# Kernel optimization log

Hardware: AMD Instinct MI355X
Metric: run time of the kernel (lower is better)

## Reference

```python
import jax, jax.numpy as jnp
import numpy as np

N = 8192
D_IN = 3
D_K = 128
HID = 256
N_RES = 2
N_TRI = 2730
N_EDGE = 2048
EPS = float(jnp.finfo(jnp.float32).eps)  # torch RMSNorm default eps=None -> finfo eps


def setup_inputs() -> dict:
    key = jax.random.key(0)
    ks = jax.random.split(key, 16)
    std = 0.02
    inp = {
        "edge_features": jax.random.normal(ks[0], (N, D_IN), dtype=jnp.float32),
        "edge_ids": jax.random.randint(ks[1], (N,), 0, N_EDGE),
        "triangle_ids": jax.random.randint(ks[2], (N,), 0, N_TRI),
        # projections (stored as [in, out]; equivalent to torch Linear)
        "Wq": jax.random.normal(ks[3], (D_IN, D_K), dtype=jnp.float32) * std,
        "bq": jnp.zeros((D_K,), jnp.float32),
        "Wk": jax.random.normal(ks[4], (D_IN, D_K), dtype=jnp.float32) * std,
        "bk": jnp.zeros((D_K,), jnp.float32),
        "Wv": jax.random.normal(ks[5], (D_IN, D_K), dtype=jnp.float32) * std,
        "bv": jnp.zeros((D_K,), jnp.float32),
        # attention MLP: Linear(d_k, hid) -> N_RES ResBlocks -> Linear(hid, 1)
        "W0": jax.random.normal(ks[6], (D_K, HID), dtype=jnp.float32) * std,
        "b0": jnp.zeros((HID,), jnp.float32),
        "rms_w": jnp.ones((N_RES, HID), jnp.float32),
        "Wres": jax.random.normal(ks[7], (N_RES, HID, HID), dtype=jnp.float32) * std,
        "bres": jnp.zeros((N_RES, HID), jnp.float32),
        "Wout": jax.random.normal(ks[8], (HID, 1), dtype=jnp.float32) * std,
        "bout": jnp.zeros((1,), jnp.float32),
    }
    return inp


def _rmsnorm(x, g):
    ms = jnp.mean(x * x, axis=-1, keepdims=True)
    return x * jax.lax.rsqrt(ms + EPS) * g


def reference(edge_features, edge_ids, triangle_ids,
              Wq, bq, Wk, bk, Wv, bv,
              W0, b0, rms_w, Wres, bres, Wout, bout):
    q = edge_features @ Wq + bq          # [N, d_k]
    k = edge_features @ Wk + bk
    v = edge_features @ Wv + bv
    scores = (q @ k.T) / jnp.sqrt(jnp.float32(D_K))   # [N, N]
    mask = triangle_ids[:, None] == triangle_ids[None, :]
    scores = jnp.where(mask, scores, -jnp.inf)
    attn = jax.nn.softmax(scores, axis=1)             # every row has diag True
    attended = attn @ v                                # [N, d_k]
    # MLP with ResBlocks
    h = attended @ W0 + b0                             # [N, hid]
    for i in range(N_RES):
        h = h + jax.nn.relu(_rmsnorm(h, rms_w[i]) @ Wres[i] + bres[i])
    logits = (h @ Wout + bout)[:, 0]                   # [N]
    # scatter_softmax over edge_ids (dim=0)
    seg_max = jax.ops.segment_max(logits, edge_ids, num_segments=N_EDGE)
    ex = jnp.exp(logits - seg_max[edge_ids])
    seg_sum = jax.ops.segment_sum(ex, edge_ids, num_segments=N_EDGE)
    weights = ex / seg_sum[edge_ids]
    return weights
```

## Files before the change

kernel.cpp:

```cpp
#include <hip/hip_runtime.h>
#include <math.h>

#define N 8192
#define D_IN 3
#define D_K 128
#define HID 256
#define N_RES 2
#define N_TRI 2730
#define N_EDGE 2048
#define EPS 1.1920929e-07f

typedef unsigned short u16;
typedef unsigned int u32;
typedef float f32x4 __attribute__((ext_vector_type(4)));
typedef short s16x8 __attribute__((ext_vector_type(8)));

#define OFF_LOGITS   0
#define OFF_TRIOFF   32768
#define OFF_TRICNT   43776
#define OFF_MEMT     54784
#define OFF_EOFF     87552
#define OFF_ECNT     95744
#define OFF_MEME     103936
#define OFF_WPK      136704

__device__ __forceinline__ u16 f2bf(float f) {
    u32 u = __float_as_uint(f);
    u32 r = (u + 0x7fffu + ((u >> 16) & 1u)) >> 16;
    return (u16)r;
}
__device__ __forceinline__ u32 pack2bf(float a, float b) {
    return (u32)f2bf(a) | ((u32)f2bf(b) << 16);
}

__global__ __launch_bounds__(1024) void k_setup(
        const int* __restrict__ tri, const int* __restrict__ eids,
        const float* __restrict__ W0, const float* __restrict__ Wres,
        int* __restrict__ tri_off, int* __restrict__ tri_cnt, int* __restrict__ mem_t,
        int* __restrict__ e_off, int* __restrict__ e_cnt, int* __restrict__ mem_e,
        u16* __restrict__ Wpk) {
    if (blockIdx.x != 0) {
        int tg = (blockIdx.x - 1) * 1024 + threadIdx.x;
        int tile = tg >> 6, lane = tg & 63;
        int q = lane >> 4, c = lane & 15;
        u16 tmp[8];
        int dst;
        if (tile < 64) {
            int nt = tile >> 2, kt = tile & 3;
            int k0 = kt * 32 + q * 8, n = nt * 16 + c;
            dst = (tile * 64 + lane) * 8;
            #pragma unroll
            for (int j = 0; j < 8; ++j) tmp[j] = f2bf(W0[(k0 + j) * HID + n]);
        } else {
            int t2 = tile - 64;
            int r = t2 >> 7, tl = t2 & 127;
            int nt = tl >> 3, kt = tl & 7;
            int k0 = kt * 32 + q * 8, n = nt * 16 + c;
            dst = 32768 + r * 65536 + (tl * 64 + lane) * 8;
            const float* W = Wres + r * 65536;
            #pragma unroll
            for (int j = 0; j < 8; ++j) tmp[j] = f2bf(W[(k0 + j) * HID + n]);
        }
        *(s16x8*)&Wpk[dst] = *(s16x8*)tmp;
        return;
    }
    __shared__ int sc[4096];
    __shared__ int ec[2048];
    __shared__ int wp[16];
    const int t = threadIdx.x, lane = t & 63, wid = t >> 6;
    for (int i = t; i < 4096; i += 1024) sc[i] = 0;
    for (int i = t; i < 2048; i += 1024) ec[i] = 0;
    __syncthreads();
    for (int n = t; n < N; n += 1024) {
        atomicAdd(&sc[tri[n]], 1);
        atomicAdd(&ec[eids[n]], 1);
    }
    __syncthreads();
    int a0 = sc[t*4], a1 = sc[t*4+1], a2 = sc[t*4+2], a3 = sc[t*4+3];
    int c0 = a0, c1 = c0 + a1, c2 = c1 + a2, c3 = c2 + a3;
    int ts = c3;
    #pragma unroll
    for (int o = 1; o < 64; o <<= 1) { int u = __shfl_up(ts, o); if (lane >= o) ts += u; }
    if (lane == 63) wp[wid] = ts;
    __syncthreads();
    if (wid == 0) {
        int v = (lane < 16) ? wp[lane] : 0;
        #pragma unroll
        for (int o = 1; o < 16; o <<= 1) { int u = __shfl_up(v, o); if (lane >= o) v += u; }
        if (lane < 16) wp[lane] = v;
    }
    __syncthreads();
    {
        int wexcl = wid ? wp[wid - 1] : 0;
        int texcl = wexcl + ts - c3;
        int o0 = texcl, o1 = texcl + c0, o2 = texcl + c1, o3 = texcl + c2;
        if (t*4+0 < N_TRI) { tri_off[t*4+0] = o0; tri_cnt[t*4+0] = a0; }
        if (t*4+1 < N_TRI) { tri_off[t*4+1] = o1; tri_cnt[t*4+1] = a1; }
        if (t*4+2 < N_TRI) { tri_off[t*4+2] = o2; tri_cnt[t*4+2] = a2; }
        if (t*4+3 < N_TRI) { tri_off[t*4+3] = o3; tri_cnt[t*4+3] = a3; }
        sc[t*4+0] = o0; sc[t*4+1] = o1; sc[t*4+2] = o2; sc[t*4+3] = o3;
    }
    __syncthreads();
    int ea0 = ec[t*2], ea1 = ec[t*2+1];
    int f0 = ea0, f1 = f0 + ea1;
    int es = f1;
    #pragma unroll
    for (int o = 1; o < 64; o <<= 1) { int u = __shfl_up(es, o); if (lane >= o) es += u; }
    if (lane == 63) wp[wid] = es;
    __syncthreads();
    if (wid == 0) {
        int v = (lane < 16) ? wp[lane] : 0;
        #pragma unroll
        for (int o = 1; o < 16; o <<= 1) { int u = __shfl_up(v, o); if (lane >= o) v += u; }
        if (lane < 16) wp[lane] = v;
    }
    __syncthreads();
    {
        int wexcl = wid ? wp[wid - 1] : 0;
        int texcl = wexcl + es - f1;
        int eo0 = texcl, eo1 = texcl + f0;
        e_off[t*2+0] = eo0; e_cnt[t*2+0] = ea0;
        e_off[t*2+1] = eo1; e_cnt[t*2+1] = ea1;
        ec[t*2+0] = eo0; ec[t*2+1] = eo1;
    }
    __syncthreads();
    for (int n = t; n < N; n += 1024) {
        int p = atomicAdd(&sc[tri[n]], 1);
        mem_t[p] = n;
        int q2 = atomicAdd(&ec[eids[n]], 1);
        mem_e[q2] = n;
    }
}

__global__ __launch_bounds__(512) void k_fused(
        const float* __restrict__ ef, const int* __restrict__ tri,
        const float* __restrict__ Wq, const float* __restrict__ bq,
        const float* __restrict__ Wk, const float* __restrict__ bk,
        const float* __restrict__ Wv, const float* __restrict__ bv,
        const int* __restrict__ tri_off, const int* __restrict__ tri_cnt,
        const int* __restrict__ mem_t,
        const float* __restrict__ b0, const float* __restrict__ rms_w,
        const float* __restrict__ bres, const float* __restrict__ Wout,
        const float* __restrict__ bout, const u16* __restrict__ Wpk,
        float* __restrict__ logits) {
    __shared__ u16 X[16][264];
    __shared__ float red[8][16];
    const int tid = threadIdx.x;
    const int w = tid >> 6, lane = tid & 63;
    const int q = lane >> 4, c = lane & 15;
    const int base = blockIdx.x * 16;
    const int colb = w * 32 + c;

    {
        const int d0 = lane * 2, d1 = d0 + 1;
        float wq0a = Wq[d0], wq1a = Wq[D_K + d0], wq2a = Wq[2*D_K + d0], bqa = bq[d0];
        float wq0b = Wq[d1], wq1b = Wq[D_K + d1], wq2b = Wq[2*D_K + d1], bqb = bq[d1];
        float wk0a = Wk[d0], wk1a = Wk[D_K + d0], wk2a = Wk[2*D_K + d0], bka = bk[d0];
        float wk0b = Wk[d1], wk1b = Wk[D_K + d1], wk2b = Wk[2*D_K + d1], bkb = bk[d1];
        float wv0a = Wv[d0], wv1a = Wv[D_K + d0], wv2a = Wv[2*D_K + d0], bva = bv[d0];
        float wv0b = Wv[d1], wv1b = Wv[D_K + d1], wv2b = Wv[2*D_K + d1], bvb = bv[d1];
        const float scale = 0.08838834764831845f;

        #pragma unroll
        for (int rr = 0; rr < 2; ++rr) {
            int lrow = 2 * w + rr;
            int row = base + lrow;
            float e0 = ef[row*3+0], e1 = ef[row*3+1], e2 = ef[row*3+2];
            float qa = bqa + e0*wq0a + e1*wq1a + e2*wq2a;
            float qb = bqb + e0*wq0b + e1*wq1b + e2*wq2b;
            int tt = tri[row];
            int off = tri_off[tt], cnt = tri_cnt[tt];
            float m = -INFINITY, l = 0.f, acca = 0.f, accb = 0.f;
            for (int bs = 0; bs < cnt; bs += 64) {
                int nn = cnt - bs; if (nn > 64) nn = 64;
                float g0 = 0.f, g1 = 0.f, g2 = 0.f;
                if (lane < nn) {
                    int j = mem_t[off + bs + lane];
                    g0 = ef[j*3+0]; g1 = ef[j*3+1]; g2 = ef[j*3+2];
                }
                for (int ii = 0; ii < nn; ++ii) {
                    float h0 = __shfl(g0, ii), h1 = __shfl(g1, ii), h2 = __shfl(g2, ii);
                    float ka = bka + h0*wk0a + h1*wk1a + h2*wk2a;
                    float kb = bkb + h0*wk0b + h1*wk1b + h2*wk2b;
                    float p = qa * ka + qb * kb;
                    #pragma unroll
                    for (int o = 32; o > 0; o >>= 1) p += __shfl_xor(p, o);
                    float s = p * scale;
                    float va = bva + h0*wv0a + h1*wv1a + h2*wv2a;
                    float vb = bvb + h0*wv0b + h1*wv1b + h2*wv2b;
                    float mn = fmaxf(m, s);
                    float rs = expf(m - mn);
                    float ws = expf(s - mn);
                    l    = l * rs + ws;
                    acca = acca * rs + ws * va;
                    accb = accb * rs + ws * vb;
                    m = mn;
                }
            }
            float inv = 1.f / l;
            *(u32*)&X[lrow][d0] = pack2bf(acca * inv, accb * inv);
        }
    }
    __syncthreads();

    const s16x8* Bp = (const s16x8*)Wpk;
    float h[2][4];
    f32x4 acc[2];
    const f32x4 zero = {0.f, 0.f, 0.f, 0.f};

    #pragma unroll
    for (int nt = 0; nt < 2; ++nt) acc[nt] = zero;
    #pragma unroll
    for (int kt = 0; kt < 4; ++kt) {
        s16x8 a = *(const s16x8*)&X[c][kt * 32 + q * 8];
        #pragma unroll
        for (int nt = 0; nt < 2; ++nt) {
            s16x8 b = Bp[((w * 2 + nt) * 4 + kt) * 64 + lane];
            acc[nt] = __builtin_amdgcn_mfma_f32_16x16x32_bf16(a, b, acc[nt], 0, 0, 0);
        }
    }
    #pragma unroll
    for (int nt = 0; nt < 2; ++nt) {
        float bb = b0[colb + nt * 16];
        #pragma unroll
        for (int rg = 0; rg < 4; ++rg) h[nt][rg] = acc[nt][rg] + bb;
    }

    for (int ir = 0; ir < N_RES; ++ir) {
        float part[4];
        #pragma unroll
        for (int rg = 0; rg < 4; ++rg) {
            part[rg] = h[0][rg] * h[0][rg] + h[1][rg] * h[1][rg];
            #pragma unroll
            for (int o = 1; o < 16; o <<= 1) part[rg] += __shfl_xor(part[rg], o);
        }
        if (c == 0) {
            #pragma unroll
            for (int rg = 0; rg < 4; ++rg) red[w][q * 4 + rg] = part[rg];
        }
        __syncthreads();
        float sc4[4];
        #pragma unroll
        for (int rg = 0; rg < 4; ++rg) {
            int rr = q * 4 + rg;
            float ms = (red[0][rr] + red[1][rr] + red[2][rr] + red[3][rr]
                      + red[4][rr] + red[5][rr] + red[6][rr] + red[7][rr]) * (1.f / HID);
            sc4[rg] = rsqrtf(ms + EPS);
        }
        #pragma unroll
        for (int nt = 0; nt < 2; ++nt) {
            float gg = rms_w[ir * HID + colb + nt * 16];
            #pragma unroll
            for (int rg = 0; rg < 4; ++rg)
                X[q * 4 + rg][colb + nt * 16] = f2bf(h[nt][rg] * sc4[rg] * gg);
        }
        __syncthreads();

        const s16x8* Br = Bp + 4096 + ir * 8192;
        #pragma unroll
        for (int nt = 0; nt < 2; ++nt) acc[nt] = zero;
        #pragma unroll
        for (int kt = 0; kt < 8; ++kt) {
            s16x8 a = *(const s16x8*)&X[c][kt * 32 + q * 8];
            #pragma unroll
            for (int nt = 0; nt < 2; ++nt) {
                s16x8 b = Br[((w * 2 + nt) * 8 + kt) * 64 + lane];
                acc[nt] = __builtin_amdgcn_mfma_f32_16x16x32_bf16(a, b, acc[nt], 0, 0, 0);
            }
        }
        #pragma unroll
        for (int nt = 0; nt < 2; ++nt) {
            float bb = bres[ir * HID + colb + nt * 16];
            #pragma unroll
            for (int rg = 0; rg < 4; ++rg) h[nt][rg] += fmaxf(acc[nt][rg] + bb, 0.f);
        }
    }

    {
        float wo0 = Wout[colb], wo1 = Wout[colb + 16];
        float part[4];
        #pragma unroll
        for (int rg = 0; rg < 4; ++rg) {
            part[rg] = h[0][rg] * wo0 + h[1][rg] * wo1;
            #pragma unroll
            for (int o = 1; o < 16; o <<= 1) part[rg] += __shfl_xor(part[rg], o);
        }
        if (c == 0) {
            #pragma unroll
            for (int rg = 0; rg < 4; ++rg) red[w][q * 4 + rg] = part[rg];
        }
        __syncthreads();
        if (tid < 16) {
            float s = bout[0];
            #pragma unroll
            for (int w2 = 0; w2 < 8; ++w2) s += red[w2][tid];
            logits[base + tid] = s;
        }
    }
}

__global__ __launch_bounds__(256) void k_segsoft(
        const float* __restrict__ logits, const int* __restrict__ e_off,
        const int* __restrict__ e_cnt, const int* __restrict__ mem_e,
        float* __restrict__ out) {
    int e = (blockIdx.x * 256 + threadIdx.x) >> 6;
    int lane = threadIdx.x & 63;
    int off = e_off[e], cnt = e_cnt[e];
    float mx = -INFINITY;
    for (int i = lane; i < cnt; i += 64) mx = fmaxf(mx, logits[mem_e[off + i]]);
    #pragma unroll
    for (int o = 32; o > 0; o >>= 1) mx = fmaxf(mx, __shfl_xor(mx, o));
    float s = 0.f;
    for (int i = lane; i < cnt; i += 64) s += expf(logits[mem_e[off + i]] - mx);
    #pragma unroll
    for (int o = 32; o > 0; o >>= 1) s += __shfl_xor(s, o);
    float inv = 1.f / s;
    for (int i = lane; i < cnt; i += 64) {
        int m = mem_e[off + i];
        out[m] = expf(logits[m] - mx) * inv;
    }
}

extern "C" void kernel_launch(void* const* d_in, const int* in_sizes, int n_in,
                              void* d_out, int out_size, void* d_ws, size_t ws_size,
                              hipStream_t stream) {
    const float* ef   = (const float*)d_in[0];
    const int*   eids = (const int*)d_in[1];
    const int*   tri  = (const int*)d_in[2];
    const float* Wq = (const float*)d_in[3];
    const float* bq = (const float*)d_in[4];
    const float* Wk = (const float*)d_in[5];
    const float* bk = (const float*)d_in[6];
    const float* Wv = (const float*)d_in[7];
    const float* bv = (const float*)d_in[8];
    const float* W0 = (const float*)d_in[9];
    const float* b0 = (const float*)d_in[10];
    const float* rms_w = (const float*)d_in[11];
    const float* Wres  = (const float*)d_in[12];
    const float* bres  = (const float*)d_in[13];
    const float* Wout  = (const float*)d_in[14];
    const float* bout  = (const float*)d_in[15];
    float* out = (float*)d_out;

    char* ws = (char*)d_ws;
    float* logits  = (float*)(ws + OFF_LOGITS);
    int*   tri_off = (int*)(ws + OFF_TRIOFF);
    int*   tri_cnt = (int*)(ws + OFF_TRICNT);
    int*   mem_t   = (int*)(ws + OFF_MEMT);
    int*   e_off   = (int*)(ws + OFF_EOFF);
    int*   e_cnt   = (int*)(ws + OFF_ECNT);
    int*   mem_e   = (int*)(ws + OFF_MEME);
    u16*   Wpk     = (u16*)(ws + OFF_WPK);

    hipLaunchKernelGGL(k_setup, dim3(21), dim3(1024), 0, stream,
                       tri, eids, W0, Wres,
                       tri_off, tri_cnt, mem_t, e_off, e_cnt, mem_e, Wpk);
    hipLaunchKernelGGL(k_fused, dim3(N / 16), dim3(512), 0, stream,
                       ef, tri, Wq, bq, Wk, bk, Wv, bv,
                       tri_off, tri_cnt, mem_t,
                       b0, rms_w, bres, Wout, bout, Wpk, logits);
    hipLaunchKernelGGL(k_segsoft, dim3(N_EDGE / 4), dim3(256), 0, stream,
                       logits, e_off, e_cnt, mem_e, out);
}
```

Before: 117.8 us.

## Double rows per block in fused MLP to reuse each weight fragment twice

The fused attention+MLP kernel now processes 32 rows per block with 1024 threads (16 waves), and each wave owns 16 output columns across two 16-row tiles instead of 32 columns for one tile. Each B (weight) fragment loaded from global memory feeds two MFMAs, which halves per-row weight traffic. The RMSNorm reduction is restructured to compute per-row scales once into shared memory, at the cost of an extra barrier. Larger blocks halve the grid size to 256 blocks, which may reduce parallelism on a many-CU device, and the attention prologue must now cover more rows per block.

```diff
diff --git a/kernel.cpp b/kernel.cpp
--- a/kernel.cpp
+++ b/kernel.cpp
@@ -132,7 +132,7 @@
     }
 }
 
-__global__ __launch_bounds__(512) void k_fused(
+__global__ __launch_bounds__(1024, 4) void k_fused(
         const float* __restrict__ ef, const int* __restrict__ tri,
         const float* __restrict__ Wq, const float* __restrict__ bq,
         const float* __restrict__ Wk, const float* __restrict__ bk,
@@ -143,13 +143,14 @@
         const float* __restrict__ bres, const float* __restrict__ Wout,
         const float* __restrict__ bout, const u16* __restrict__ Wpk,
         float* __restrict__ logits) {
-    __shared__ u16 X[16][264];
-    __shared__ float red[8][16];
+    __shared__ u16 X[32][264];
+    __shared__ float red[16][32];
+    __shared__ float srow[32];
     const int tid = threadIdx.x;
     const int w = tid >> 6, lane = tid & 63;
     const int q = lane >> 4, c = lane & 15;
-    const int base = blockIdx.x * 16;
-    const int colb = w * 32 + c;
+    const int base = blockIdx.x * 32;
+    const int colb = w * 16 + c;
 
     {
         const int d0 = lane * 2, d1 = d0 + 1;
@@ -205,95 +206,93 @@
 
     const s16x8* Bp = (const s16x8*)Wpk;
     float h[2][4];
-    f32x4 acc[2];
     const f32x4 zero = {0.f, 0.f, 0.f, 0.f};
 
-    #pragma unroll
-    for (int nt = 0; nt < 2; ++nt) acc[nt] = zero;
-    #pragma unroll
-    for (int kt = 0; kt < 4; ++kt) {
-        s16x8 a = *(const s16x8*)&X[c][kt * 32 + q * 8];
-        #pragma unroll
-        for (int nt = 0; nt < 2; ++nt) {
-            s16x8 b = Bp[((w * 2 + nt) * 4 + kt) * 64 + lane];
-            acc[nt] = __builtin_amdgcn_mfma_f32_16x16x32_bf16(a, b, acc[nt], 0, 0, 0);
-        }
-    }
-    #pragma unroll
-    for (int nt = 0; nt < 2; ++nt) {
-        float bb = b0[colb + nt * 16];
-        #pragma unroll
-        for (int rg = 0; rg < 4; ++rg) h[nt][rg] = acc[nt][rg] + bb;
+    {
+        f32x4 acc0 = zero, acc1 = zero;
+        #pragma unroll
+        for (int kt = 0; kt < 4; ++kt) {
+            s16x8 b  = Bp[(w * 4 + kt) * 64 + lane];
+            s16x8 a0 = *(const s16x8*)&X[c][kt * 32 + q * 8];
+            s16x8 a1 = *(const s16x8*)&X[16 + c][kt * 32 + q * 8];
+            acc0 = __builtin_amdgcn_mfma_f32_16x16x32_bf16(a0, b, acc0, 0, 0, 0);
+            acc1 = __builtin_amdgcn_mfma_f32_16x16x32_bf16(a1, b, acc1, 0, 0, 0);
+        }
+        float bb = b0[colb];
+        #pragma unroll
+        for (int rg = 0; rg < 4; ++rg) { h[0][rg] = acc0[rg] + bb; h[1][rg] = acc1[rg] + bb; }
     }
 
     for (int ir = 0; ir < N_RES; ++ir) {
-        float part[4];
+        float part[2][4];
+        #pragma unroll
+        for (int rt = 0; rt < 2; ++rt)
+            #pragma unroll
+            for (int rg = 0; rg < 4; ++rg) {
+                float v = h[rt][rg] * h[rt][rg];
+                #pragma unroll
+                for (int o = 1; o < 16; o <<= 1) v += __shfl_xor(v, o);
+                part[rt][rg] = v;
+            }
+        if (c == 0) {
+            #pragma unroll
+            for (int rt = 0; rt < 2; ++rt)
+                #pragma unroll
+                for (int rg = 0; rg < 4; ++rg)
+                    red[w][rt * 16 + q * 4 + rg] = part[rt][rg];
+        }
+        __syncthreads();
+        if (tid < 32) {
+            float s = 0.f;
+            #pragma unroll
+            for (int w2 = 0; w2 < 16; ++w2) s += red[w2][tid];
+            srow[tid] = rsqrtf(s * (1.f / HID) + EPS);
+        }
+        __syncthreads();
+        float gg = rms_w[ir * HID + colb];
+        #pragma unroll
+        for (int rt = 0; rt < 2; ++rt)
+            #pragma unroll
+            for (int rg = 0; rg < 4; ++rg) {
+                int rr = rt * 16 + q * 4 + rg;
+                X[rr][colb] = f2bf(h[rt][rg] * srow[rr] * gg);
+            }
+        __syncthreads();
+
+        const s16x8* Br = Bp + 4096 + ir * 8192;
+        f32x4 acc0 = zero, acc1 = zero;
+        #pragma unroll
+        for (int kt = 0; kt < 8; ++kt) {
+            s16x8 b  = Br[(w * 8 + kt) * 64 + lane];
+            s16x8 a0 = *(const s16x8*)&X[c][kt * 32 + q * 8];
+            s16x8 a1 = *(const s16x8*)&X[16 + c][kt * 32 + q * 8];
+            acc0 = __builtin_amdgcn_mfma_f32_16x16x32_bf16(a0, b, acc0, 0, 0, 0);
+            acc1 = __builtin_amdgcn_mfma_f32_16x16x32_bf16(a1, b, acc1, 0, 0, 0);
+        }
+        float bb = bres[ir * HID + colb];
         #pragma unroll
         for (int rg = 0; rg < 4; ++rg) {
-            part[rg] = h[0][rg] * h[0][rg] + h[1][rg] * h[1][rg];
-            #pragma unroll
-            for (int o = 1; o < 16; o <<= 1) part[rg] += __shfl_xor(part[rg], o);
-        }
-        if (c == 0) {
-            #pragma unroll
-            for (int rg = 0; rg < 4; ++rg) red[w][q * 4 + rg] = part[rg];
-        }
+            h[0][rg] += fmaxf(acc0[rg] + bb, 0.f);
+            h[1][rg] += fmaxf(acc1[rg] + bb, 0.f);
+        }
+    }
+
+    {
+        float wo = Wout[colb];
+        #pragma unroll
+        for (int rt = 0; rt < 2; ++rt)
+            #pragma unroll
+            for (int rg = 0; rg < 4; ++rg) {
+                float v = h[rt][rg] * wo;
+                #pragma unroll
+                for (int o = 1; o < 16; o <<= 1) v += __shfl_xor(v, o);
+                if (c == 0) red[w][rt * 16 + q * 4 + rg] = v;
+            }
         __syncthreads();
-        float sc4[4];
-        #pragma unroll
-        for (int rg = 0; rg < 4; ++rg) {
-            int rr = q * 4 + rg;
-            float ms = (red[0][rr] + red[1][rr] + red[2][rr] + red[3][rr]
-                      + red[4][rr] + red[5][rr] + red[6][rr] + red[7][rr]) * (1.f / HID);
-            sc4[rg] = rsqrtf(ms + EPS);
-        }
-        #pragma unroll
-        for (int nt = 0; nt < 2; ++nt) {
-            float gg = rms_w[ir * HID + colb + nt * 16];
-            #pragma unroll
-            for (int rg = 0; rg < 4; ++rg)
-                X[q * 4 + rg][colb + nt * 16] = f2bf(h[nt][rg] * sc4[rg] * gg);
-        }
-        __syncthreads();
-
-        const s16x8* Br = Bp + 4096 + ir * 8192;
-        #pragma unroll
-        for (int nt = 0; nt < 2; ++nt) acc[nt] = zero;
-        #pragma unroll
-        for (int kt = 0; kt < 8; ++kt) {
-            s16x8 a = *(const s16x8*)&X[c][kt * 32 + q * 8];
-            #pragma unroll
-            for (int nt = 0; nt < 2; ++nt) {
-                s16x8 b = Br[((w * 2 + nt) * 8 + kt) * 64 + lane];
-                acc[nt] = __builtin_amdgcn_mfma_f32_16x16x32_bf16(a, b, acc[nt], 0, 0, 0);
-            }
-        }
-        #pragma unroll
-        for (int nt = 0; nt < 2; ++nt) {
-            float bb = bres[ir * HID + colb + nt * 16];
-            #pragma unroll
-            for (int rg = 0; rg < 4; ++rg) h[nt][rg] += fmaxf(acc[nt][rg] + bb, 0.f);
-        }
-    }
-
-    {
-        float wo0 = Wout[colb], wo1 = Wout[colb + 16];
-        float part[4];
-        #pragma unroll
-        for (int rg = 0; rg < 4; ++rg) {
-            part[rg] = h[0][rg] * wo0 + h[1][rg] * wo1;
-            #pragma unroll
-            for (int o = 1; o < 16; o <<= 1) part[rg] += __shfl_xor(part[rg], o);
-        }
-        if (c == 0) {
-            #pragma unroll
-            for (int rg = 0; rg < 4; ++rg) red[w][q * 4 + rg] = part[rg];
-        }
-        __syncthreads();
-        if (tid < 16) {
+        if (tid < 32) {
             float s = bout[0];
             #pragma unroll
-            for (int w2 = 0; w2 < 8; ++w2) s += red[w2][tid];
+            for (int w2 = 0; w2 < 16; ++w2) s += red[w2][tid];
             logits[base + tid] = s;
         }
     }
@@ -355,7 +354,7 @@
     hipLaunchKernelGGL(k_setup, dim3(21), dim3(1024), 0, stream,
                        tri, eids, W0, Wres,
                        tri_off, tri_cnt, mem_t, e_off, e_cnt, mem_e, Wpk);
-    hipLaunchKernelGGL(k_fused, dim3(N / 16), dim3(512), 0, stream,
+    hipLaunchKernelGGL(k_fused, dim3(N / 32), dim3(1024), 0, stream,
                        ef, tri, Wq, bq, Wk, bk, Wv, bv,
                        tri_off, tri_cnt, mem_t,
                        b0, rms_w, bres, Wout, bout, Wpk, logits);
```

Measured after the change: 121.9 us. +3.5%, slower.
